# Optimization experiments

Measured on AMD Instinct MI355X. Metric: run time of the kernel, lower is better.

## Reference

```python
import jax, jax.numpy as jnp
import numpy as np


def _haar_dwt2(x):
    # x: [b, H, W] -> (ll, lh, hl, hh), each [b, H/2, W/2]; orthonormal 2D Haar
    a = x[:, ::2, ::2]
    b = x[:, ::2, 1::2]
    c = x[:, 1::2, ::2]
    d = x[:, 1::2, 1::2]
    ll = (a + b + c + d) * 0.5
    lh = (a + b - c - d) * 0.5  # detail along rows (frames)
    hl = (a - b + c - d) * 0.5  # detail along cols (features)
    hh = (a - b - c + d) * 0.5
    return ll, lh, hl, hh


def _haar_idwt2(ll, lh, hl, hh):
    a = (ll + lh + hl + hh) * 0.5
    b = (ll + lh - hl - hh) * 0.5
    c = (ll - lh + hl - hh) * 0.5
    d = (ll - lh - hl + hh) * 0.5
    B, H2, W2 = ll.shape
    out = jnp.zeros((B, 2 * H2, 2 * W2), ll.dtype)
    out = out.at[:, ::2, ::2].set(a)
    out = out.at[:, ::2, 1::2].set(b)
    out = out.at[:, 1::2, ::2].set(c)
    out = out.at[:, 1::2, 1::2].set(d)
    return out


def _interp_linear_last(x, m):
    # linear interpolation along last dim from linspace(0,1,n) to linspace(0,1,m)
    n = x.shape[-1]
    pos = jnp.linspace(0.0, 1.0, m, dtype=x.dtype) * (n - 1)
    i0 = jnp.clip(jnp.floor(pos).astype(jnp.int32), 0, n - 2)
    w = pos - i0.astype(x.dtype)
    return x[..., i0] * (1.0 - w) + x[..., i0 + 1] * w


def setup_inputs() -> dict:
    key = jax.random.key(0)
    k0, k1, k2 = jax.random.split(key, 3)
    b, f, c, hidden = 128, 256, 512, 2048
    x = jax.random.normal(k0, (b, f, c), dtype=jnp.float32)
    fc1_w = jax.random.normal(k1, (hidden, c), dtype=jnp.float32) * 0.02
    fc1_b = jnp.zeros((hidden,), dtype=jnp.float32)
    fc2_w = jax.random.normal(k2, (c // 2, hidden), dtype=jnp.float32) * 0.02
    fc2_b = jnp.zeros((c // 2,), dtype=jnp.float32)
    return {"x": x, "fc1_w": fc1_w, "fc1_b": fc1_b, "fc2_w": fc2_w, "fc2_b": fc2_b}


def reference(x, fc1_w, fc1_b, fc2_w, fc2_b):
    b, f, c = x.shape
    ll, lh, hl, hh = _haar_dwt2(x)               # [b, f/2, c/2] each
    ll_up = _interp_linear_last(ll, c)           # [b, f/2, c]
    h = jax.nn.gelu(jnp.einsum('bfc,hc->bfh', ll_up, fc1_w) + fc1_b, approximate=False)
    ll_new = jnp.einsum('bfh,oh->bfo', h, fc2_w) + fc2_b  # [b, f/2, c/2]
    return _haar_idwt2(ll_new, lh, hl, hh)       # [b, f, c]
```

## Files before the change

### kernel.cpp

```cpp
#include <hip/hip_runtime.h>
#include <hip/hip_bf16.h>
#include <stdint.h>

typedef __bf16 bf16;
typedef __attribute__((ext_vector_type(8))) __bf16 bf16x8;
typedef __attribute__((ext_vector_type(4))) float f32x4;

#define B_DIM 128
#define F_DIM 256
#define C_DIM 512
#define HID   2048
#define F2    (F_DIM/2)
#define C2    (C_DIM/2)
#define MROWS (B_DIM*F2)

static constexpr size_t OFF_W1P = 0;
static constexpr size_t OFF_W2  = OFF_W1P + (size_t)HID * C2 * 2;

__device__ __forceinline__ unsigned short bfbits(float f) {
    bf16 h = (bf16)f;
    return __builtin_bit_cast(unsigned short, h);
}

typedef const __attribute__((address_space(1))) unsigned int as1_uint;
typedef __attribute__((address_space(3))) unsigned int as3_uint;
__device__ __forceinline__ void gld_lds16(const void* g, void* l) {
    as1_uint* gp = (as1_uint*)(uintptr_t)g;
    as3_uint* lp = (as3_uint*)(uintptr_t)l;
    __builtin_amdgcn_global_load_lds(gp, lp, 16, 0, 0);
}

#define VMCNT2() asm volatile("s_waitcnt vmcnt(2)" ::: "memory")
#define VMCNT0() asm volatile("s_waitcnt vmcnt(0)" ::: "memory")

__global__ __launch_bounds__(256) void prep_kernel(
    const float* __restrict__ w1, const float* __restrict__ w2,
    ushort* __restrict__ w1p, ushort* __restrict__ w2b)
{
    const int blk = blockIdx.x;
    const int t = threadIdx.x;
    if (blk < 2048) {
        int idx = blk * 256 + t;
        int h = idx >> 8, i = idx & 255;
        const float* wrow = w1 + (size_t)h * C_DIM;
        float acc = 0.f;
        int jlo = (i == 0) ? 0 : (int)((float)(i - 1) * (511.0f / 255.0f));
        int jhi = (int)((float)(i + 1) * (511.0f / 255.0f)) + 1;
        if (jhi > 511) jhi = 511;
        for (int j = jlo; j <= jhi; ++j) {
            float pos = (float)j * (255.0f / 511.0f);
            int i0 = (int)pos;
            if (i0 > 254) i0 = 254;
            float w = pos - (float)i0;
            float coef = (i0 == i) ? (1.0f - w) : ((i0 + 1 == i) ? w : 0.0f);
            acc += coef * wrow[j];
        }
        w1p[(size_t)h * C2 + i] = bfbits(acc);
    } else {
        int idx = (blk - 2048) * 256 + t;
        float4 v = ((const float4*)w2)[idx];
        ushort4 u;
        u.x = bfbits(v.x); u.y = bfbits(v.y); u.z = bfbits(v.z); u.w = bfbits(v.w);
        ((ushort4*)w2b)[idx] = u;
    }
}

__global__ __launch_bounds__(512, 4) void fused_mlp(
    const bf16* __restrict__ w1p, const bf16* __restrict__ w2b,
    const float* __restrict__ b1, const float* __restrict__ b2,
    const float* __restrict__ x, float* __restrict__ out)
{
    __shared__ __align__(16) char smem[65536];
    bf16* Bst0 = (bf16*)(smem + 32768);
    bf16* Bst1 = (bf16*)(smem + 49152);

    const int tid = threadIdx.x;
    const int l   = tid & 63;
    const int wv  = tid >> 6;
    const int wm  = wv >> 2;
    const int wn  = wv & 3;
    const int lr  = l & 15;
    const int q   = l >> 4;
    const int R0  = blockIdx.x * 32;
    const int e7  = lr & 7;
    const int qb  = ((q ^ (lr & 3)) << 4);

    auto stageB1 = [&](int hc, int t, bf16* buf) {
#pragma unroll
        for (int i = 0; i < 2; ++i) {
            int c = i * 512 + tid; int r = c >> 2; int sl = (c & 3) ^ (r & 3);
            gld_lds16(w1p + (size_t)(hc * 256 + r) * 256 + t * 32 + sl * 8,
                      (char*)buf + c * 16);
        }
    };
    auto stageB2 = [&](int hc, int t, bf16* buf) {
#pragma unroll
        for (int i = 0; i < 2; ++i) {
            int c = i * 512 + tid; int r = c >> 2; int sl = (c & 3) ^ (r & 3);
            gld_lds16(w2b + (size_t)r * 2048 + hc * 256 + t * 32 + sl * 8,
                      (char*)buf + c * 16);
        }
    };

    stageB1(0, 0, Bst0);

#pragma unroll
    for (int k = 0; k < 16; ++k) {
        int o = tid + k * 512;
        int r = o >> 8, c2 = o & 255;
        int gbf = R0 + r;
        const float* xr = x + ((size_t)(gbf >> 7) * F_DIM + (size_t)(gbf & 127) * 2) * C_DIM;
        float2 p0 = ((const float2*)xr)[c2];
        float2 p1 = ((const float2*)(xr + C_DIM))[c2];
        float v = 0.5f * (p0.x + p0.y + p1.x + p1.y);
        int by = (r * 512 + c2 * 2) ^ ((r & 7) << 4);
        *(bf16*)(smem + by) = (bf16)v;
    }
    __syncthreads();

    f32x4 acc2[4];
#pragma unroll
    for (int n = 0; n < 4; ++n) acc2[n] = (f32x4){0.f, 0.f, 0.f, 0.f};

    for (int hc = 0; hc < 8; ++hc) {
        f32x4 acc1[4];
#pragma unroll
        for (int n = 0; n < 4; ++n) acc1[n] = (f32x4){0.f, 0.f, 0.f, 0.f};

#pragma unroll
        for (int t = 0; t < 8; ++t) {
            bf16* cur = (t & 1) ? Bst1 : Bst0;
            if (t < 7) stageB1(hc, t + 1, (t & 1) ? Bst0 : Bst1);
            else       stageB2(hc, 0, Bst0);
            VMCNT2();
            __builtin_amdgcn_s_barrier();
            __builtin_amdgcn_sched_barrier(0);
            bf16x8 af = *(const bf16x8*)(smem +
                ((wm * 16 + lr) * 512 + ((((t << 2) + q) ^ e7) << 4)));
            bf16x8 bfr[4];
#pragma unroll
            for (int n = 0; n < 4; ++n)
                bfr[n] = *(const bf16x8*)((char*)cur + ((wn * 64 + n * 16 + lr) * 64 + qb));
#pragma unroll
            for (int n = 0; n < 4; ++n)
                acc1[n] = __builtin_amdgcn_mfma_f32_16x16x32_bf16(af, bfr[n], acc1[n], 0, 0, 0);
            __builtin_amdgcn_sched_barrier(0);
            __builtin_amdgcn_s_barrier();
        }

#pragma unroll
        for (int n = 0; n < 4; ++n) {
            int col = wn * 64 + n * 16 + lr;
            float bs = b1[hc * 256 + col];
#pragma unroll
            for (int j = 0; j < 4; ++j) {
                float v = acc1[n][j] + bs;
                float tt = v * (0.79788456080f + 0.03567740814f * v * v);
                float e = __expf(-2.0f * tt);
                float g = v / (1.0f + e);
                int row = wm * 16 + q * 4 + j;
                int by = 16384 + ((row * 512 + col * 2) ^ ((row & 7) << 4));
                *(bf16*)(smem + by) = (bf16)g;
            }
        }
        __syncthreads();

#pragma unroll
        for (int t = 0; t < 8; ++t) {
            bf16* cur = (t & 1) ? Bst1 : Bst0;
            if (t < 7)          stageB2(hc, t + 1, (t & 1) ? Bst0 : Bst1);
            else if (hc < 7)    stageB1(hc + 1, 0, Bst0);
            if (t == 7 && hc == 7) { VMCNT0(); } else { VMCNT2(); }
            __builtin_amdgcn_s_barrier();
            __builtin_amdgcn_sched_barrier(0);
            bf16x8 af = *(const bf16x8*)(smem + 16384 +
                ((wm * 16 + lr) * 512 + ((((t << 2) + q) ^ e7) << 4)));
            bf16x8 bfr[4];
#pragma unroll
            for (int n = 0; n < 4; ++n)
                bfr[n] = *(const bf16x8*)((char*)cur + ((wn * 64 + n * 16 + lr) * 64 + qb));
#pragma unroll
            for (int n = 0; n < 4; ++n)
                acc2[n] = __builtin_amdgcn_mfma_f32_16x16x32_bf16(af, bfr[n], acc2[n], 0, 0, 0);
            __builtin_amdgcn_sched_barrier(0);
            __builtin_amdgcn_s_barrier();
        }
    }

#pragma unroll
    for (int n = 0; n < 4; ++n) {
        int c2 = wn * 64 + n * 16 + lr;
        float bs = b2[c2];
#pragma unroll
        for (int j = 0; j < 4; ++j) {
            int gbf = R0 + wm * 16 + q * 4 + j;
            int b = gbf >> 7, f2 = gbf & 127;
            const float* xr = x + ((size_t)b * F_DIM + (size_t)f2 * 2) * C_DIM;
            float2 p0 = ((const float2*)xr)[c2];
            float2 p1 = ((const float2*)(xr + C_DIM))[c2];
            float a = p0.x, bb = p0.y, cc = p1.x, dd = p1.y;
            float llv = acc2[n][j] + bs;
            float lh = 0.5f * (a + bb - cc - dd);
            float hl = 0.5f * (a - bb + cc - dd);
            float hh = 0.5f * (a - bb - cc + dd);
            float2 o0, o1;
            o0.x = 0.5f * (llv + lh + hl + hh);
            o0.y = 0.5f * (llv + lh - hl - hh);
            o1.x = 0.5f * (llv - lh + hl - hh);
            o1.y = 0.5f * (llv - lh - hl + hh);
            float* orow = out + ((size_t)b * F_DIM + (size_t)f2 * 2) * C_DIM;
            ((float2*)orow)[c2] = o0;
            ((float2*)(orow + C_DIM))[c2] = o1;
        }
    }
}

extern "C" void kernel_launch(void* const* d_in, const int* in_sizes, int n_in,
                              void* d_out, int out_size, void* d_ws, size_t ws_size,
                              hipStream_t stream) {
    const float* x     = (const float*)d_in[0];
    const float* fc1_w = (const float*)d_in[1];
    const float* fc1_b = (const float*)d_in[2];
    const float* fc2_w = (const float*)d_in[3];
    const float* fc2_b = (const float*)d_in[4];
    float* out = (float*)d_out;

    char* ws = (char*)d_ws;
    bf16* w1p = (bf16*)(ws + OFF_W1P);
    bf16* w2b = (bf16*)(ws + OFF_W2);

    prep_kernel<<<2560, 256, 0, stream>>>(fc1_w, fc2_w, (ushort*)w1p, (ushort*)w2b);
    fused_mlp<<<MROWS / 32, 512, 0, stream>>>(w1p, w2b, fc1_b, fc2_b, x, out);
}
```

Measured before the change: 107.6 us.

## Pre-pack weights into MFMA fragment order and load them directly from global memory

The prep kernel now writes fc1 and fc2 weights in a fragment-packed layout, so each lane can load its 16-byte MFMA B operand straight from global memory. This removes LDS staging, the double buffering and the per-step barriers. Warps are re-split so each of the 8 waves covers all 32 rows and 32 output columns, with 2x2 MFMA tiles that reuse each loaded weight fragment twice. The costs are that global weight loads are now exposed with no explicit prefetch, the prep kernel does scattered scalar writes, and A fragments are reloaded from LDS by every wave.

```diff
diff --git a/kernel.cpp b/kernel.cpp
--- a/kernel.cpp
+++ b/kernel.cpp
@@ -22,195 +22,179 @@
     return __builtin_bit_cast(unsigned short, h);
 }
 
-typedef const __attribute__((address_space(1))) unsigned int as1_uint;
-typedef __attribute__((address_space(3))) unsigned int as3_uint;
-__device__ __forceinline__ void gld_lds16(const void* g, void* l) {
-    as1_uint* gp = (as1_uint*)(uintptr_t)g;
-    as3_uint* lp = (as3_uint*)(uintptr_t)l;
-    __builtin_amdgcn_global_load_lds(gp, lp, 16, 0, 0);
-}
-
-#define VMCNT2() asm volatile("s_waitcnt vmcnt(2)" ::: "memory")
-#define VMCNT0() asm volatile("s_waitcnt vmcnt(0)" ::: "memory")
-
 __global__ __launch_bounds__(256) void prep_kernel(
     const float* __restrict__ w1, const float* __restrict__ w2,
-    ushort* __restrict__ w1p, ushort* __restrict__ w2b)
+    bf16* __restrict__ w1pp, bf16* __restrict__ w2pp)
 {
     const int blk = blockIdx.x;
     const int t = threadIdx.x;
     if (blk < 2048) {
         int idx = blk * 256 + t;
-        int h = idx >> 8, i = idx & 255;
+        int h = idx >> 8, k = idx & 255;
         const float* wrow = w1 + (size_t)h * C_DIM;
         float acc = 0.f;
-        int jlo = (i == 0) ? 0 : (int)((float)(i - 1) * (511.0f / 255.0f));
-        int jhi = (int)((float)(i + 1) * (511.0f / 255.0f)) + 1;
+        int jlo = (k == 0) ? 0 : (int)((float)(k - 1) * (511.0f / 255.0f));
+        int jhi = (int)((float)(k + 1) * (511.0f / 255.0f)) + 1;
         if (jhi > 511) jhi = 511;
         for (int j = jlo; j <= jhi; ++j) {
             float pos = (float)j * (255.0f / 511.0f);
             int i0 = (int)pos;
             if (i0 > 254) i0 = 254;
             float w = pos - (float)i0;
-            float coef = (i0 == i) ? (1.0f - w) : ((i0 + 1 == i) ? w : 0.0f);
+            float coef = (i0 == k) ? (1.0f - w) : ((i0 + 1 == k) ? w : 0.0f);
             acc += coef * wrow[j];
         }
-        w1p[(size_t)h * C2 + i] = bfbits(acc);
+        size_t off = ((((size_t)(h >> 4)) * 8 + (k >> 5)) * 64
+                      + ((((k >> 3) & 3) << 4) | (h & 15))) * 8 + (k & 7);
+        w1pp[off] = (bf16)acc;
     } else {
-        int idx = (blk - 2048) * 256 + t;
-        float4 v = ((const float4*)w2)[idx];
-        ushort4 u;
-        u.x = bfbits(v.x); u.y = bfbits(v.y); u.z = bfbits(v.z); u.w = bfbits(v.w);
-        ((ushort4*)w2b)[idx] = u;
+        int idx2 = (blk - 2048) * 256 + t;
+        int c2 = idx2 >> 11, h = idx2 & 2047;
+        float v = w2[(size_t)c2 * HID + h];
+        size_t off = ((((size_t)(c2 >> 4)) * 64 + (h >> 5)) * 64
+                      + ((((h >> 3) & 3) << 4) | (c2 & 15))) * 8 + (h & 7);
+        w2pp[off] = (bf16)v;
     }
 }
 
 __global__ __launch_bounds__(512, 4) void fused_mlp(
-    const bf16* __restrict__ w1p, const bf16* __restrict__ w2b,
+    const bf16* __restrict__ w1pp, const bf16* __restrict__ w2pp,
     const float* __restrict__ b1, const float* __restrict__ b2,
     const float* __restrict__ x, float* __restrict__ out)
 {
-    __shared__ __align__(16) char smem[65536];
-    bf16* Bst0 = (bf16*)(smem + 32768);
-    bf16* Bst1 = (bf16*)(smem + 49152);
+    __shared__ __align__(16) char smem[32768];
 
     const int tid = threadIdx.x;
     const int l   = tid & 63;
-    const int wv  = tid >> 6;
-    const int wm  = wv >> 2;
-    const int wn  = wv & 3;
+    const int wn  = tid >> 6;
     const int lr  = l & 15;
     const int q   = l >> 4;
     const int R0  = blockIdx.x * 32;
-    const int e7  = lr & 7;
-    const int qb  = ((q ^ (lr & 3)) << 4);
-
-    auto stageB1 = [&](int hc, int t, bf16* buf) {
-#pragma unroll
-        for (int i = 0; i < 2; ++i) {
-            int c = i * 512 + tid; int r = c >> 2; int sl = (c & 3) ^ (r & 3);
-            gld_lds16(w1p + (size_t)(hc * 256 + r) * 256 + t * 32 + sl * 8,
-                      (char*)buf + c * 16);
-        }
-    };
-    auto stageB2 = [&](int hc, int t, bf16* buf) {
-#pragma unroll
-        for (int i = 0; i < 2; ++i) {
-            int c = i * 512 + tid; int r = c >> 2; int sl = (c & 3) ^ (r & 3);
-            gld_lds16(w2b + (size_t)r * 2048 + hc * 256 + t * 32 + sl * 8,
-                      (char*)buf + c * 16);
-        }
-    };
-
-    stageB1(0, 0, Bst0);
-
-#pragma unroll
-    for (int k = 0; k < 16; ++k) {
-        int o = tid + k * 512;
-        int r = o >> 8, c2 = o & 255;
-        int gbf = R0 + r;
+
+    {
+        const int rr = tid >> 4;
+        const int w0 = tid & 15;
+        const int gbf = R0 + rr;
         const float* xr = x + ((size_t)(gbf >> 7) * F_DIM + (size_t)(gbf & 127) * 2) * C_DIM;
-        float2 p0 = ((const float2*)xr)[c2];
-        float2 p1 = ((const float2*)(xr + C_DIM))[c2];
-        float v = 0.5f * (p0.x + p0.y + p1.x + p1.y);
-        int by = (r * 512 + c2 * 2) ^ ((r & 7) << 4);
-        *(bf16*)(smem + by) = (bf16)v;
+        const float* xs = xr + C_DIM;
+#pragma unroll
+        for (int half = 0; half < 2; ++half) {
+            const int w = w0 + half * 16;
+            float4 ra[4], rb[4];
+#pragma unroll
+            for (int i = 0; i < 4; ++i) {
+                ra[i] = ((const float4*)xr)[w * 4 + i];
+                rb[i] = ((const float4*)xs)[w * 4 + i];
+            }
+            const float* pa = (const float*)ra;
+            const float* pb = (const float*)rb;
+            bf16x8 pk;
+#pragma unroll
+            for (int e = 0; e < 8; ++e)
+                pk[e] = (bf16)(0.5f * (pa[2*e] + pa[2*e+1] + pb[2*e] + pb[2*e+1]));
+            int slot = (((rr >> 4) * 8 + (w >> 2)) * 64) + ((w & 3) << 4) + (rr & 15);
+            *(bf16x8*)(smem + slot * 16) = pk;
+        }
     }
     __syncthreads();
 
-    f32x4 acc2[4];
-#pragma unroll
-    for (int n = 0; n < 4; ++n) acc2[n] = (f32x4){0.f, 0.f, 0.f, 0.f};
+    f32x4 acc2[2][2];
+#pragma unroll
+    for (int m = 0; m < 2; ++m)
+#pragma unroll
+        for (int n = 0; n < 2; ++n)
+            acc2[m][n] = (f32x4){0.f, 0.f, 0.f, 0.f};
 
     for (int hc = 0; hc < 8; ++hc) {
-        f32x4 acc1[4];
-#pragma unroll
-        for (int n = 0; n < 4; ++n) acc1[n] = (f32x4){0.f, 0.f, 0.f, 0.f};
+        f32x4 acc1[2][2];
+#pragma unroll
+        for (int m = 0; m < 2; ++m)
+#pragma unroll
+            for (int n = 0; n < 2; ++n)
+                acc1[m][n] = (f32x4){0.f, 0.f, 0.f, 0.f};
 
 #pragma unroll
         for (int t = 0; t < 8; ++t) {
-            bf16* cur = (t & 1) ? Bst1 : Bst0;
-            if (t < 7) stageB1(hc, t + 1, (t & 1) ? Bst0 : Bst1);
-            else       stageB2(hc, 0, Bst0);
-            VMCNT2();
-            __builtin_amdgcn_s_barrier();
-            __builtin_amdgcn_sched_barrier(0);
-            bf16x8 af = *(const bf16x8*)(smem +
-                ((wm * 16 + lr) * 512 + ((((t << 2) + q) ^ e7) << 4)));
-            bf16x8 bfr[4];
-#pragma unroll
-            for (int n = 0; n < 4; ++n)
-                bfr[n] = *(const bf16x8*)((char*)cur + ((wn * 64 + n * 16 + lr) * 64 + qb));
-#pragma unroll
-            for (int n = 0; n < 4; ++n)
-                acc1[n] = __builtin_amdgcn_mfma_f32_16x16x32_bf16(af, bfr[n], acc1[n], 0, 0, 0);
-            __builtin_amdgcn_sched_barrier(0);
-            __builtin_amdgcn_s_barrier();
-        }
-
-#pragma unroll
-        for (int n = 0; n < 4; ++n) {
-            int col = wn * 64 + n * 16 + lr;
-            float bs = b1[hc * 256 + col];
+            bf16x8 af[2];
+#pragma unroll
+            for (int m = 0; m < 2; ++m)
+                af[m] = *(const bf16x8*)(smem + ((m * 8 + t) * 64 + l) * 16);
+#pragma unroll
+            for (int n = 0; n < 2; ++n) {
+                const int hblk = hc * 16 + wn * 2 + n;
+                bf16x8 bw = *(const bf16x8*)(w1pp + (((size_t)hblk * 8 + t) * 64 + l) * 8);
+#pragma unroll
+                for (int m = 0; m < 2; ++m)
+                    acc1[m][n] = __builtin_amdgcn_mfma_f32_16x16x32_bf16(af[m], bw, acc1[m][n], 0, 0, 0);
+            }
+        }
+
+#pragma unroll
+        for (int n = 0; n < 2; ++n) {
+            const int col = wn * 32 + n * 16 + lr;
+            const float bs = b1[hc * 256 + col];
+            const int t2 = col >> 5, qq = (col >> 3) & 3, e = col & 7;
+#pragma unroll
+            for (int m = 0; m < 2; ++m) {
+#pragma unroll
+                for (int j = 0; j < 4; ++j) {
+                    float v = acc1[m][n][j] + bs;
+                    float tt = v * (0.79788456080f + 0.03567740814f * v * v);
+                    float ex = __expf(-2.0f * tt);
+                    float g = v / (1.0f + ex);
+                    const int row = m * 16 + q * 4 + j;
+                    int off = ((m * 8 + t2) * 64 + (qq << 4) + (row & 15)) * 8 + e;
+                    *(bf16*)(smem + 16384 + off * 2) = (bf16)g;
+                }
+            }
+        }
+        __syncthreads();
+
+#pragma unroll
+        for (int t = 0; t < 8; ++t) {
+            bf16x8 af[2];
+#pragma unroll
+            for (int m = 0; m < 2; ++m)
+                af[m] = *(const bf16x8*)(smem + 16384 + ((m * 8 + t) * 64 + l) * 16);
+#pragma unroll
+            for (int n = 0; n < 2; ++n) {
+                const int c2blk = wn * 2 + n;
+                bf16x8 bw = *(const bf16x8*)(w2pp + (((size_t)c2blk * 64 + hc * 8 + t) * 64 + l) * 8);
+#pragma unroll
+                for (int m = 0; m < 2; ++m)
+                    acc2[m][n] = __builtin_amdgcn_mfma_f32_16x16x32_bf16(af[m], bw, acc2[m][n], 0, 0, 0);
+            }
+        }
+        __syncthreads();
+    }
+
+#pragma unroll
+    for (int n = 0; n < 2; ++n) {
+        const int c2 = wn * 32 + n * 16 + lr;
+        const float bs = b2[c2];
+#pragma unroll
+        for (int m = 0; m < 2; ++m) {
 #pragma unroll
             for (int j = 0; j < 4; ++j) {
-                float v = acc1[n][j] + bs;
-                float tt = v * (0.79788456080f + 0.03567740814f * v * v);
-                float e = __expf(-2.0f * tt);
-                float g = v / (1.0f + e);
-                int row = wm * 16 + q * 4 + j;
-                int by = 16384 + ((row * 512 + col * 2) ^ ((row & 7) << 4));
-                *(bf16*)(smem + by) = (bf16)g;
-            }
-        }
-        __syncthreads();
-
-#pragma unroll
-        for (int t = 0; t < 8; ++t) {
-            bf16* cur = (t & 1) ? Bst1 : Bst0;
-            if (t < 7)          stageB2(hc, t + 1, (t & 1) ? Bst0 : Bst1);
-            else if (hc < 7)    stageB1(hc + 1, 0, Bst0);
-            if (t == 7 && hc == 7) { VMCNT0(); } else { VMCNT2(); }
-            __builtin_amdgcn_s_barrier();
-            __builtin_amdgcn_sched_barrier(0);
-            bf16x8 af = *(const bf16x8*)(smem + 16384 +
-                ((wm * 16 + lr) * 512 + ((((t << 2) + q) ^ e7) << 4)));
-            bf16x8 bfr[4];
-#pragma unroll
-            for (int n = 0; n < 4; ++n)
-                bfr[n] = *(const bf16x8*)((char*)cur + ((wn * 64 + n * 16 + lr) * 64 + qb));
-#pragma unroll
-            for (int n = 0; n < 4; ++n)
-                acc2[n] = __builtin_amdgcn_mfma_f32_16x16x32_bf16(af, bfr[n], acc2[n], 0, 0, 0);
-            __builtin_amdgcn_sched_barrier(0);
-            __builtin_amdgcn_s_barrier();
-        }
-    }
-
-#pragma unroll
-    for (int n = 0; n < 4; ++n) {
-        int c2 = wn * 64 + n * 16 + lr;
-        float bs = b2[c2];
-#pragma unroll
-        for (int j = 0; j < 4; ++j) {
-            int gbf = R0 + wm * 16 + q * 4 + j;
-            int b = gbf >> 7, f2 = gbf & 127;
-            const float* xr = x + ((size_t)b * F_DIM + (size_t)f2 * 2) * C_DIM;
-            float2 p0 = ((const float2*)xr)[c2];
-            float2 p1 = ((const float2*)(xr + C_DIM))[c2];
-            float a = p0.x, bb = p0.y, cc = p1.x, dd = p1.y;
-            float llv = acc2[n][j] + bs;
-            float lh = 0.5f * (a + bb - cc - dd);
-            float hl = 0.5f * (a - bb + cc - dd);
-            float hh = 0.5f * (a - bb - cc + dd);
-            float2 o0, o1;
-            o0.x = 0.5f * (llv + lh + hl + hh);
-            o0.y = 0.5f * (llv + lh - hl - hh);
-            o1.x = 0.5f * (llv - lh + hl - hh);
-            o1.y = 0.5f * (llv - lh - hl + hh);
-            float* orow = out + ((size_t)b * F_DIM + (size_t)f2 * 2) * C_DIM;
-            ((float2*)orow)[c2] = o0;
-            ((float2*)(orow + C_DIM))[c2] = o1;
+                const int gbf = R0 + m * 16 + q * 4 + j;
+                const int b = gbf >> 7, f2 = gbf & 127;
+                const float* xr = x + ((size_t)b * F_DIM + (size_t)f2 * 2) * C_DIM;
+                float2 p0 = ((const float2*)xr)[c2];
+                float2 p1 = ((const float2*)(xr + C_DIM))[c2];
+                float a = p0.x, bb = p0.y, cc = p1.x, dd = p1.y;
+                float llv = acc2[m][n][j] + bs;
+                float lh = 0.5f * (a + bb - cc - dd);
+                float hl = 0.5f * (a - bb + cc - dd);
+                float hh = 0.5f * (a - bb - cc + dd);
+                float2 o0, o1;
+                o0.x = 0.5f * (llv + lh + hl + hh);
+                o0.y = 0.5f * (llv + lh - hl - hh);
+                o1.x = 0.5f * (llv - lh + hl - hh);
+                o1.y = 0.5f * (llv - lh - hl + hh);
+                float* orow = out + ((size_t)b * F_DIM + (size_t)f2 * 2) * C_DIM;
+                ((float2*)orow)[c2] = o0;
+                ((float2*)(orow + C_DIM))[c2] = o1;
+            }
         }
     }
 }
@@ -226,9 +210,9 @@
     float* out = (float*)d_out;
 
     char* ws = (char*)d_ws;
-    bf16* w1p = (bf16*)(ws + OFF_W1P);
-    bf16* w2b = (bf16*)(ws + OFF_W2);
-
-    prep_kernel<<<2560, 256, 0, stream>>>(fc1_w, fc2_w, (ushort*)w1p, (ushort*)w2b);
-    fused_mlp<<<MROWS / 32, 512, 0, stream>>>(w1p, w2b, fc1_b, fc2_b, x, out);
-}
+    bf16* w1pp = (bf16*)(ws + OFF_W1P);
+    bf16* w2pp = (bf16*)(ws + OFF_W2);
+
+    prep_kernel<<<4096, 256, 0, stream>>>(fc1_w, fc2_w, w1pp, w2pp);
+    fused_mlp<<<MROWS / 32, 512, 0, stream>>>(w1pp, w2pp, fc1_b, fc2_b, x, out);
+}
```

Result: faster. 99.94 us (-7.1%).
